# Optimization experiments

Measured on AMD Instinct MI355X. Metric: run time of the kernel, lower is better.

The kernel has to match this reference:

```python
import jax, jax.numpy as jnp
import numpy as np

N_NODES = 20000
N_EDGES = 40000
N_GRAPHS = 800
NODE_DIM = 64
EDGE_DIM = 16
ATOM = 64
CONV_DIM = 128
NUM_EMBEDS = 3   # message-passing rounds
EMB_STEPS = 3    # Set2Set processing steps
MLP1, MLP2, OUT = 512, 256, 34
BN_EPS = 1e-5


def setup_inputs() -> dict:
    key = jax.random.key(0)
    ks = jax.random.split(key, 16)
    nrm = lambda k, shape, s: jax.random.normal(k, shape, jnp.float32) * s
    inp = {}
    inp["x_feat"] = nrm(ks[0], (N_NODES, NODE_DIM), 1.0)
    inp["edge_attr"] = nrm(ks[1], (N_EDGES, EDGE_DIM), 1.0)
    inp["edge_index"] = jax.random.randint(ks[2], (2, N_EDGES), 0, N_NODES, dtype=jnp.int32)
    # sorted graph assignment; every graph non-empty (~25 nodes each)
    inp["batch"] = (jnp.arange(N_NODES) * N_GRAPHS // N_NODES).astype(jnp.int32)
    # linatoms
    inp["W_lin"] = nrm(ks[3], (NODE_DIM, ATOM), 0.1); inp["b_lin"] = jnp.zeros((ATOM,), jnp.float32)
    # edge MLP: edge_dim -> conv_dim -> atom_dim^2
    inp["W_e1"] = nrm(ks[4], (EDGE_DIM, CONV_DIM), 0.1); inp["b_e1"] = jnp.zeros((CONV_DIM,), jnp.float32)
    inp["W_e2"] = nrm(ks[5], (CONV_DIM, ATOM * ATOM), 0.02); inp["b_e2"] = jnp.zeros((ATOM * ATOM,), jnp.float32)
    inp["b_conv"] = jnp.zeros((ATOM,), jnp.float32)  # NNConv bias (root_weight=False)
    # GRU (PyTorch layout: (3*H, in), gates [r, z, n])
    inp["gru_Wih"] = nrm(ks[6], (3 * ATOM, ATOM), 0.1); inp["gru_Whh"] = nrm(ks[7], (3 * ATOM, ATOM), 0.1)
    inp["gru_bih"] = jnp.zeros((3 * ATOM,), jnp.float32); inp["gru_bhh"] = jnp.zeros((3 * ATOM,), jnp.float32)
    # Set2Set LSTM (input 2*d, hidden d; gates [i, f, g, o])
    inp["lstm_Wih"] = nrm(ks[8], (4 * ATOM, 2 * ATOM), 0.1); inp["lstm_Whh"] = nrm(ks[9], (4 * ATOM, ATOM), 0.1)
    inp["lstm_bih"] = jnp.zeros((4 * ATOM,), jnp.float32); inp["lstm_bhh"] = jnp.zeros((4 * ATOM,), jnp.float32)
    # BatchNorm1d(2*atom_dim)
    inp["bn_gamma"] = jnp.ones((2 * ATOM,), jnp.float32); inp["bn_beta"] = jnp.zeros((2 * ATOM,), jnp.float32)
    # MLP + pred head
    inp["W_m1"] = nrm(ks[10], (2 * ATOM, MLP1), 0.05); inp["b_m1"] = jnp.zeros((MLP1,), jnp.float32)
    inp["W_m2"] = nrm(ks[11], (MLP1, MLP2), 0.05); inp["b_m2"] = jnp.zeros((MLP2,), jnp.float32)
    inp["W_p"] = nrm(ks[12], (MLP2, OUT), 0.05); inp["b_p"] = jnp.zeros((OUT,), jnp.float32)
    return inp


def _forward(x_feat, edge_attr, edge_index, batch,
             W_lin, b_lin, W_e1, b_e1, W_e2, b_e2, b_conv,
             gru_Wih, gru_Whh, gru_bih, gru_bhh,
             lstm_Wih, lstm_Whh, lstm_bih, lstm_bhh,
             bn_gamma, bn_beta, W_m1, b_m1, W_m2, b_m2, W_p, b_p):
    d = ATOM
    src, dst = edge_index[0], edge_index[1]

    x = jax.nn.relu(x_feat @ W_lin + b_lin)          # [N, d]
    h = x                                            # GRU hidden state

    # edge MLP -> per-edge [d, d] weight matrices (edge_attr is constant across rounds)
    W_edges = (jax.nn.relu(edge_attr @ W_e1 + b_e1) @ W_e2 + b_e2).reshape(N_EDGES, d, d)

    deg = jax.ops.segment_sum(jnp.ones((N_EDGES,), jnp.float32), dst, num_segments=N_NODES)
    deg = jnp.maximum(deg, 1.0)[:, None]             # mean aggregation

    for _ in range(NUM_EMBEDS):
        msg = jnp.einsum('ed,edf->ef', x[src], W_edges)               # per-edge matmul
        agg = jax.ops.segment_sum(msg, dst, num_segments=N_NODES) / deg
        m = jax.nn.relu(agg + b_conv)
        # GRU cell (seq_len=1): gates ordered [r, z, n]
        gi = m @ gru_Wih.T + gru_bih
        gh = h @ gru_Whh.T + gru_bhh
        r = jax.nn.sigmoid(gi[:, :d] + gh[:, :d])
        z = jax.nn.sigmoid(gi[:, d:2 * d] + gh[:, d:2 * d])
        n = jnp.tanh(gi[:, 2 * d:] + r * gh[:, 2 * d:])
        h = (1.0 - z) * n + z * h
        x = h

    # Set2Set pooling: [N, d] -> [B, 2d]
    B = N_GRAPHS
    q_star = jnp.zeros((B, 2 * d), x.dtype)
    hl = jnp.zeros((B, d), x.dtype)
    cl = jnp.zeros((B, d), x.dtype)
    for _ in range(EMB_STEPS):
        g = q_star @ lstm_Wih.T + lstm_bih + hl @ lstm_Whh.T + lstm_bhh
        i_g = jax.nn.sigmoid(g[:, :d])
        f_g = jax.nn.sigmoid(g[:, d:2 * d])
        c_g = jnp.tanh(g[:, 2 * d:3 * d])
        o_g = jax.nn.sigmoid(g[:, 3 * d:])
        cl = f_g * cl + i_g * c_g
        hl = o_g * jnp.tanh(cl)
        q = hl                                                       # [B, d]
        e = jnp.sum(x * q[batch], axis=-1)                           # [N]
        emax = jax.ops.segment_max(e, batch, num_segments=B)
        ee = jnp.exp(e - emax[batch])
        zden = jax.ops.segment_sum(ee, batch, num_segments=B)
        a = ee / zden[batch]                                         # per-graph softmax
        r_read = jax.ops.segment_sum(a[:, None] * x, batch, num_segments=B)
        q_star = jnp.concatenate([q, r_read], axis=-1)

    # BatchNorm1d (training-mode batch stats)
    mu = jnp.mean(q_star, axis=0)
    var = jnp.var(q_star, axis=0)
    y = bn_gamma * (q_star - mu) / jnp.sqrt(var + BN_EPS) + bn_beta

    y = jax.nn.relu(y @ W_m1 + b_m1)
    y = jax.nn.relu(y @ W_m2 + b_m2)
    return y @ W_p + b_p                                             # [B, 34]


def reference(x_feat, edge_attr, edge_index, batch,
              W_lin, b_lin, W_e1, b_e1, W_e2, b_e2, b_conv,
              gru_Wih, gru_Whh, gru_bih, gru_bhh,
              lstm_Wih, lstm_Whh, lstm_bih, lstm_bhh,
              bn_gamma, bn_beta, W_m1, b_m1, W_m2, b_m2, W_p, b_p):
    return _forward(x_feat, edge_attr, edge_index, batch,
                    W_lin, b_lin, W_e1, b_e1, W_e2, b_e2, b_conv,
                    gru_Wih, gru_Whh, gru_bih, gru_bhh,
                    lstm_Wih, lstm_Whh, lstm_bih, lstm_bhh,
                    bn_gamma, bn_beta, W_m1, b_m1, W_m2, b_m2, W_p, b_p)
```

## Files before the change

### kernel.cpp

```cpp
#include <hip/hip_runtime.h>
#include <hip/hip_bf16.h>
#include <cstdint>
#include <cstddef>

#define N_NODES 20000
#define N_EDGES 40000
#define EPAD 40192
#define N_GRAPHS 800
#define ATOM 64
#define MLP1D 512
#define MLP2D 256
#define NOUT 34

typedef _Float16 h2 __attribute__((ext_vector_type(2)));
typedef _Float16 half8 __attribute__((ext_vector_type(8)));
typedef float f32x4 __attribute__((ext_vector_type(4)));
typedef float f32x16 __attribute__((ext_vector_type(16)));

__device__ __forceinline__ float sigm(float x) { return 1.f / (1.f + expf(-x)); }

#define LIN_BLKS 5000
#define HEP_BLKS (EPAD / 64)
#define BF_TOTAL (129 * 4096)
#define BF_BLKS ((BF_TOTAL + 255) / 256)
#define MISC_TOTAL (12288 + 12288 + 32768 + 16384 + EPAD + (N_GRAPHS + 1) + N_EDGES)
#define MISC_BLKS ((MISC_TOTAL + 255) / 256)
#define PREP_BLKS (LIN_BLKS + HEP_BLKS + BF_BLKS + MISC_BLKS)

__global__ __launch_bounds__(256) void prep_all(
    const float* __restrict__ x_feat, const float* __restrict__ W_lin,
    const float* __restrict__ b_lin, float* __restrict__ hx, _Float16* __restrict__ xh,
    const float* __restrict__ ea, const float* __restrict__ W_e1,
    const float* __restrict__ b_e1, _Float16* __restrict__ heT,
    const float* __restrict__ We2, const float* __restrict__ be2, _Float16* __restrict__ Bg,
    const float* __restrict__ gWih, const float* __restrict__ gWhh,
    const float* __restrict__ lWih, const float* __restrict__ lWhh,
    _Float16* __restrict__ gWihT, _Float16* __restrict__ gWhhT,
    _Float16* __restrict__ lWihT, _Float16* __restrict__ lWhhT,
    const int* __restrict__ batch, int* __restrict__ gstart,
    const int* __restrict__ dst, float* __restrict__ deg) {
    int bx = blockIdx.x;
    if (bx < LIN_BLKS) {
        __shared__ float xr[4][64];
        int ln = threadIdx.x >> 6, j = threadIdx.x & 63;
        int n = (bx << 2) + ln;
        xr[ln][j] = x_feat[(size_t)n * 64 + j];
        __syncthreads();
        float acc = b_lin[j];
        for (int i = 0; i < 64; ++i) acc = fmaf(xr[ln][i], W_lin[i * 64 + j], acc);
        float r = fmaxf(acc, 0.f);
        hx[(size_t)n * 64 + j] = r;
        xh[(size_t)n * 64 + j] = (_Float16)r;
        return;
    }
    bx -= LIN_BLKS;
    if (bx < HEP_BLKS) {
        __shared__ float eaL[64 * 17];
        int e0 = bx * 64;
        for (int idx = threadIdx.x; idx < 1024; idx += 256) {
            int r = idx >> 4, i = idx & 15;
            int e = e0 + r;
            eaL[r * 17 + i] = (e < N_EDGES) ? ea[(size_t)e * 16 + i] : 0.f;
        }
        __syncthreads();
        int w = threadIdx.x >> 6, lane = threadIdx.x & 63;
        for (int c = w; c < 128; c += 4) {
            float acc = b_e1[c];
            #pragma unroll
            for (int i = 0; i < 16; ++i)
                acc = fmaf(eaL[lane * 17 + i], W_e1[i * 128 + c], acc);
            heT[(size_t)c * EPAD + e0 + lane] = (_Float16)fmaxf(acc, 0.f);
        }
        return;
    }
    bx -= HEP_BLKS;
    if (bx < BF_BLKS) {
        int idx = bx * 256 + threadIdx.x;
        if (idx >= BF_TOTAL) return;
        int j = idx & 7, lane = (idx >> 3) & 63, ft = (idx >> 9) & 1;
        int kc = (idx >> 10) & 3, c = idx >> 12;
        int k = kc * 16 + (lane >> 5) * 8 + j;
        int f = ft * 32 + (lane & 31);
        float v = (c < 128) ? We2[(size_t)c * 4096 + k * 64 + f] : be2[k * 64 + f];
        Bg[idx] = (_Float16)v;
        return;
    }
    bx -= BF_BLKS;
    {
        int i = bx * 256 + threadIdx.x;
        if (i < 12288) { int r = i / 64, c = i % 64; gWihT[c * 192 + r] = (_Float16)gWih[i]; return; }
        i -= 12288;
        if (i < 12288) { int r = i / 64, c = i % 64; gWhhT[c * 192 + r] = (_Float16)gWhh[i]; return; }
        i -= 12288;
        if (i < 32768) { int r = i / 128, c = i % 128; lWihT[c * 256 + r] = (_Float16)lWih[i]; return; }
        i -= 32768;
        if (i < 16384) { int r = i / 64, c = i % 64; lWhhT[c * 256 + r] = (_Float16)lWhh[i]; return; }
        i -= 16384;
        if (i < EPAD) { heT[(size_t)128 * EPAD + i] = (_Float16)1.0f; return; }
        i -= EPAD;
        if (i <= N_GRAPHS) {
            if (i == N_GRAPHS) { gstart[i] = N_NODES; return; }
            int lo = 0, hi = N_NODES;
            while (lo < hi) { int mid = (lo + hi) >> 1; if (batch[mid] < i) lo = mid + 1; else hi = mid; }
            gstart[i] = lo;
            return;
        }
        i -= (N_GRAPHS + 1);
        if (i < N_EDGES) { atomicAdd(&deg[dst[i]], 1.f); return; }
    }
}

__global__ __launch_bounds__(256) void msg_v10(
    const _Float16* __restrict__ Bg, const _Float16* __restrict__ heT,
    const _Float16* __restrict__ xh, const int* __restrict__ src,
    const int* __restrict__ dst, float* __restrict__ agg)
{
    int tid = threadIdx.x;
    int w = tid >> 6, lane = tid & 63;
    int l5 = lane >> 5, l31 = lane & 31;
    int bx = blockIdx.x;
    int ft = bx & 1;
    int eg = bx >> 1;
    int m0 = eg * 128 + w * 32;
    int KS = gridDim.y, ks = blockIdx.y;
    int c0 = (129 * ks) / KS;
    int c1 = (129 * (ks + 1)) / KS;
    int nc = c1 - c0;

    union XU { h2 p[4]; half8 v; } xf[4];
    {
        int e = m0 + l31;
        const _Float16* xp = xh + (size_t)src[e] * 64 + l5 * 8;
        xf[0].v = *(const half8*)(xp);
        xf[1].v = *(const half8*)(xp + 16);
        xf[2].v = *(const half8*)(xp + 32);
        xf[3].v = *(const half8*)(xp + 48);
    }

    f32x16 acc = {};
    const _Float16* bbase = Bg + ft * 512 + lane * 8;
    const _Float16* hbase = heT + m0 + l31;

    half8 bA[4], bB[4];
    _Float16 hA, hB;

    auto LOADB = [&](int c, half8* bb, _Float16& hh) {
        const _Float16* bp = bbase + c * 4096;
        bb[0] = *(const half8*)(bp);
        bb[1] = *(const half8*)(bp + 1024);
        bb[2] = *(const half8*)(bp + 2048);
        bb[3] = *(const half8*)(bp + 3072);
        hh = hbase[c * EPAD];
    };
    auto COMP = [&](const half8* bb, _Float16 hh) {
        h2 hv = (h2){hh, hh};
        #pragma unroll
        for (int kc = 0; kc < 4; ++kc) {
            union XU a;
            #pragma unroll
            for (int j = 0; j < 4; ++j) a.p[j] = hv * xf[kc].p[j];
            acc = __builtin_amdgcn_mfma_f32_32x32x16_f16(a.v, bb[kc], acc, 0, 0, 0);
        }
    };

    int cur = bx % nc;
    LOADB(c0 + cur, bA, hA);
    int done = 1;
    for (; done + 1 < nc; done += 2) {
        int n1 = (cur + 1 == nc) ? 0 : cur + 1;
        LOADB(c0 + n1, bB, hB);
        COMP(bA, hA);
        int n2 = (n1 + 1 == nc) ? 0 : n1 + 1;
        LOADB(c0 + n2, bA, hA);
        COMP(bB, hB);
        cur = n2;
    }
    if (done < nc) {
        int n1 = (cur + 1 == nc) ? 0 : cur + 1;
        LOADB(c0 + n1, bB, hB);
        COMP(bA, hA);
        COMP(bB, hB);
    } else {
        COMP(bA, hA);
    }

    int fc = ft * 32 + l31;
    #pragma unroll
    for (int r = 0; r < 16; ++r) {
        int e = m0 + (r & 3) + 8 * (r >> 2) + 4 * l5;
        if (e < N_EDGES)
            atomicAdd(&agg[(size_t)dst[e] * 64 + fc], acc[r]);
    }
}

__global__ __launch_bounds__(256) void gru_kernel(float* __restrict__ agg,
    const float* __restrict__ deg, const float* __restrict__ bconv,
    const _Float16* __restrict__ WihT, const _Float16* __restrict__ WhhT,
    const float* __restrict__ bih, const float* __restrict__ bhh,
    float* __restrict__ hx, _Float16* __restrict__ xh) {
    __shared__ float mh[4][2][64];
    int ln = threadIdx.x >> 6, j = threadIdx.x & 63;
    int n = (blockIdx.x << 2) + ln;
    float dg = fmaxf(deg[n], 1.f);
    size_t idx = (size_t)n * 64 + j;
    float m = fmaxf(agg[idx] / dg + bconv[j], 0.f);
    agg[idx] = 0.f;
    float h = hx[idx];
    mh[ln][0][j] = m; mh[ln][1][j] = h;
    __syncthreads();
    float gri = bih[j], gzi = bih[64 + j], gni = bih[128 + j];
    float grh = bhh[j], gzh = bhh[64 + j], gnh = bhh[128 + j];
    for (int i = 0; i < 64; ++i) {
        float mi = mh[ln][0][i], hi = mh[ln][1][i];
        gri = fmaf(mi, (float)WihT[i * 192 + j], gri);
        gzi = fmaf(mi, (float)WihT[i * 192 + 64 + j], gzi);
        gni = fmaf(mi, (float)WihT[i * 192 + 128 + j], gni);
        grh = fmaf(hi, (float)WhhT[i * 192 + j], grh);
        gzh = fmaf(hi, (float)WhhT[i * 192 + 64 + j], gzh);
        gnh = fmaf(hi, (float)WhhT[i * 192 + 128 + j], gnh);
    }
    float rr = sigm(gri + grh);
    float zz = sigm(gzi + gzh);
    float nn = tanhf(gni + rr * gnh);
    float hnew = (1.f - zz) * nn + zz * h;
    hx[idx] = hnew;
    xh[idx] = (_Float16)hnew;
}

__global__ __launch_bounds__(256) void s2s_kernel(const float* __restrict__ x,
    const int* __restrict__ gstart,
    const _Float16* __restrict__ WI,
    const _Float16* __restrict__ WH,
    const float* __restrict__ bih, const float* __restrict__ bhh,
    float* __restrict__ qstar) {
    __shared__ float st[192];
    __shared__ float gl[256];
    __shared__ float redmax[4], redsum[4];
    __shared__ float raccs[4][64];
    int g = blockIdx.x, t = threadIdx.x;
    int w = t >> 6, j = t & 63;
    int s0 = gstart[g], s1 = gstart[g + 1];
    if (t < 192) st[t] = 0.f;
    float cj = 0.f;
    float bsum = bih[t] + bhh[t];
    __syncthreads();
    for (int s = 0; s < 3; ++s) {
        float a0 = bsum, a1 = 0.f;
        #pragma unroll 8
        for (int i = 0; i < 128; i += 2) {
            a0 = fmaf(st[i], (float)WI[i * 256 + t], a0);
            a1 = fmaf(st[i + 1], (float)WI[(i + 1) * 256 + t], a1);
        }
        #pragma unroll 8
        for (int i = 0; i < 64; i += 2) {
            a0 = fmaf(st[128 + i], (float)WH[i * 256 + t], a0);
            a1 = fmaf(st[128 + i + 1], (float)WH[(i + 1) * 256 + t], a1);
        }
        gl[t] = a0 + a1;
        __syncthreads();
        if (t < 64) {
            float ig = sigm(gl[t]);
            float fg = sigm(gl[64 + t]);
            float cg = tanhf(gl[128 + t]);
            float og = sigm(gl[192 + t]);
            cj = fg * cj + ig * cg;
            float hnew = og * tanhf(cj);
            st[t] = hnew;
            st[128 + t] = hnew;
        }
        __syncthreads();
        float hj = st[128 + j];
        float pmax = -3.0e38f;
        for (int n = s0 + w; n < s1; n += 4) {
            float v = x[(size_t)n * 64 + j] * hj;
            for (int o = 32; o; o >>= 1) v += __shfl_xor(v, o);
            pmax = fmaxf(pmax, v);
        }
        if (j == 0) redmax[w] = pmax;
        __syncthreads();
        float emax = fmaxf(fmaxf(redmax[0], redmax[1]), fmaxf(redmax[2], redmax[3]));
        float esum = 0.f, racc = 0.f;
        for (int n = s0 + w; n < s1; n += 4) {
            float xv = x[(size_t)n * 64 + j];
            float v = xv * hj;
            for (int o = 32; o; o >>= 1) v += __shfl_xor(v, o);
            float ww = expf(v - emax);
            esum += ww;
            racc = fmaf(ww, xv, racc);
        }
        raccs[w][j] = racc;
        if (j == 0) redsum[w] = esum;
        __syncthreads();
        if (t < 64) {
            float es = redsum[0] + redsum[1] + redsum[2] + redsum[3];
            st[64 + j] = (raccs[0][j] + raccs[1][j] + raccs[2][j] + raccs[3][j]) / es;
        }
        __syncthreads();
    }
    if (t < 64) {
        qstar[g * 128 + t] = st[t];
        qstar[g * 128 + 64 + t] = st[64 + t];
    }
}

__global__ void bn_kernel(const float* __restrict__ qs, const float* __restrict__ gamma,
                          const float* __restrict__ beta, float* __restrict__ out) {
    int c = blockIdx.x, l = threadIdx.x;
    float s = 0.f, ss = 0.f;
    for (int r = l; r < N_GRAPHS; r += 64) {
        float v = qs[r * 128 + c];
        s += v; ss += v * v;
    }
    for (int o = 32; o; o >>= 1) { s += __shfl_xor(s, o); ss += __shfl_xor(ss, o); }
    float mu = s * (1.f / N_GRAPHS);
    float var = ss * (1.f / N_GRAPHS) - mu * mu;
    float inv = rsqrtf(var + 1e-5f);
    float ga = gamma[c], be = beta[c];
    for (int r = l; r < N_GRAPHS; r += 64)
        out[r * 128 + c] = ga * (qs[r * 128 + c] - mu) * inv + be;
}

__global__ __launch_bounds__(512) void head_fused(const float* __restrict__ bno,
    const float* __restrict__ Wm1, const float* __restrict__ bm1,
    const float* __restrict__ Wm2, const float* __restrict__ bm2,
    const float* __restrict__ Wp, const float* __restrict__ bp,
    float* __restrict__ out) {
    __shared__ float row[128];
    __shared__ float y1[512];
    __shared__ float y2[256];
    int g = blockIdx.x, t = threadIdx.x;
    int rot = (g * 17) & 127;
    if (t < 128) row[t] = bno[g * 128 + t];
    __syncthreads();
    float acc = bm1[t];
    for (int s = 0; s < 128; ++s) {
        int i = (s + rot) & 127;
        acc = fmaf(row[i], Wm1[i * MLP1D + t], acc);
    }
    y1[t] = fmaxf(acc, 0.f);
    __syncthreads();
    if (t < 256) {
        float a2 = bm2[t];
        int rot2 = (g * 31) & 511;
        for (int s = 0; s < 512; ++s) {
            int i = (s + rot2) & 511;
            a2 = fmaf(y1[i], Wm2[i * MLP2D + t], a2);
        }
        y2[t] = fmaxf(a2, 0.f);
    }
    __syncthreads();
    if (t < NOUT) {
        float a3 = bp[t];
        int rot3 = (g * 13) & 255;
        for (int s = 0; s < 256; ++s) {
            int i = (s + rot3) & 255;
            a3 = fmaf(y2[i], Wp[i * NOUT + t], a3);
        }
        out[g * NOUT + t] = a3;
    }
}

extern "C" void kernel_launch(void* const* d_in, const int* in_sizes, int n_in,
                              void* d_out, int out_size, void* d_ws, size_t ws_size,
                              hipStream_t stream) {
    (void)in_sizes; (void)n_in; (void)out_size; (void)ws_size;
    const float* x_feat    = (const float*)d_in[0];
    const float* edge_attr = (const float*)d_in[1];
    const int*   eidx      = (const int*)d_in[2];
    const int*   batch     = (const int*)d_in[3];
    const float* W_lin = (const float*)d_in[4];
    const float* b_lin = (const float*)d_in[5];
    const float* W_e1  = (const float*)d_in[6];
    const float* b_e1  = (const float*)d_in[7];
    const float* W_e2  = (const float*)d_in[8];
    const float* b_e2  = (const float*)d_in[9];
    const float* b_conv= (const float*)d_in[10];
    const float* gWih  = (const float*)d_in[11];
    const float* gWhh  = (const float*)d_in[12];
    const float* gbih  = (const float*)d_in[13];
    const float* gbhh  = (const float*)d_in[14];
    const float* lWih  = (const float*)d_in[15];
    const float* lWhh  = (const float*)d_in[16];
    const float* lbih  = (const float*)d_in[17];
    const float* lbhh  = (const float*)d_in[18];
    const float* bng   = (const float*)d_in[19];
    const float* bnb   = (const float*)d_in[20];
    const float* Wm1   = (const float*)d_in[21];
    const float* bm1   = (const float*)d_in[22];
    const float* Wm2   = (const float*)d_in[23];
    const float* bm2   = (const float*)d_in[24];
    const float* Wp    = (const float*)d_in[25];
    const float* bp    = (const float*)d_in[26];
    float* out = (float*)d_out;

    const int* src = eidx;
    const int* dst = eidx + N_EDGES;

    char* w = (char*)d_ws;
    size_t off = 0;
    auto alloc = [&](size_t bytes) -> char* {
        char* p = w + off; off += (bytes + 255) & ~(size_t)255; return p;
    };
    _Float16* Bg     = (_Float16*)alloc((size_t)129 * 4096 * 2);
    _Float16* heT    = (_Float16*)alloc((size_t)129 * EPAD * 2);
    _Float16* xh     = (_Float16*)alloc((size_t)N_NODES * 64 * 2);
    float* hx        = (float*)alloc((size_t)N_NODES * 64 * 4);
    float* agg       = (float*)alloc((size_t)N_NODES * 64 * 4);
    float* deg       = (float*)alloc((size_t)N_NODES * 4);
    _Float16* gWihT  = (_Float16*)alloc(192 * 64 * 2);
    _Float16* gWhhT  = (_Float16*)alloc(192 * 64 * 2);
    _Float16* lWihT  = (_Float16*)alloc(256 * 128 * 2);
    _Float16* lWhhT  = (_Float16*)alloc(256 * 64 * 2);
    float* qstar     = (float*)alloc((size_t)N_GRAPHS * 128 * 4);
    int*   gst       = (int*)alloc((N_GRAPHS + 1) * 4);
    float* bno       = (float*)alloc((size_t)N_GRAPHS * 128 * 4);

    hipMemsetAsync(agg, 0, (size_t)N_NODES * 64 * 4 + (size_t)N_NODES * 4, stream);

    prep_all<<<PREP_BLKS, 256, 0, stream>>>(
        x_feat, W_lin, b_lin, hx, xh,
        edge_attr, W_e1, b_e1, heT,
        W_e2, b_e2, Bg,
        gWih, gWhh, lWih, lWhh, gWihT, gWhhT, lWihT, lWhhT,
        batch, gst, dst, deg);

    for (int r = 0; r < 3; ++r) {
        msg_v10<<<dim3(628, 2), 256, 0, stream>>>(Bg, heT, xh, src, dst, agg);
        gru_kernel<<<N_NODES / 4, 256, 0, stream>>>(agg, deg, b_conv, gWihT, gWhhT, gbih, gbhh, hx, xh);
    }

    s2s_kernel<<<N_GRAPHS, 256, 0, stream>>>(hx, gst, lWihT, lWhhT, lbih, lbhh, qstar);

    bn_kernel<<<128, 64, 0, stream>>>(qstar, bng, bnb, bno);
    head_fused<<<N_GRAPHS, 512, 0, stream>>>(bno, Wm1, bm1, Wm2, bm2, Wp, bp, out);
}
```

Baseline: 471.8 us.

## Restructure GRU to one thread per gate row across four nodes with fp32 float4 weights

```diff
diff --git a/kernel.cpp b/kernel.cpp
--- a/kernel.cpp
+++ b/kernel.cpp
@@ -35,8 +35,8 @@
     const float* __restrict__ We2, const float* __restrict__ be2, _Float16* __restrict__ Bg,
     const float* __restrict__ gWih, const float* __restrict__ gWhh,
     const float* __restrict__ lWih, const float* __restrict__ lWhh,
-    _Float16* __restrict__ gWihT, _Float16* __restrict__ gWhhT,
-    _Float16* __restrict__ lWihT, _Float16* __restrict__ lWhhT,
+    float* __restrict__ gWih4, float* __restrict__ gWhh4,
+    float* __restrict__ lWih4, float* __restrict__ lWhh4,
     const int* __restrict__ batch, int* __restrict__ gstart,
     const int* __restrict__ dst, float* __restrict__ deg) {
     int bx = blockIdx.x;
@@ -88,13 +88,17 @@
     bx -= BF_BLKS;
     {
         int i = bx * 256 + threadIdx.x;
-        if (i < 12288) { int r = i / 64, c = i % 64; gWihT[c * 192 + r] = (_Float16)gWih[i]; return; }
+        if (i < 12288) { int j = i & 3; int rest = i >> 2; int t = rest % 192; int ib = rest / 192;
+                         gWih4[i] = gWih[t * 64 + ib * 4 + j]; return; }
         i -= 12288;
-        if (i < 12288) { int r = i / 64, c = i % 64; gWhhT[c * 192 + r] = (_Float16)gWhh[i]; return; }
+        if (i < 12288) { int j = i & 3; int rest = i >> 2; int t = rest % 192; int ib = rest / 192;
+                         gWhh4[i] = gWhh[t * 64 + ib * 4 + j]; return; }
         i -= 12288;
-        if (i < 32768) { int r = i / 128, c = i % 128; lWihT[c * 256 + r] = (_Float16)lWih[i]; return; }
+        if (i < 32768) { int j = i & 3; int rest = i >> 2; int t = rest & 255; int ib = rest >> 8;
+                         lWih4[i] = lWih[t * 128 + ib * 4 + j]; return; }
         i -= 32768;
-        if (i < 16384) { int r = i / 64, c = i % 64; lWhhT[c * 256 + r] = (_Float16)lWhh[i]; return; }
+        if (i < 16384) { int j = i & 3; int rest = i >> 2; int t = rest & 255; int ib = rest >> 8;
+                         lWhh4[i] = lWhh[t * 64 + ib * 4 + j]; return; }
         i -= 16384;
         if (i < EPAD) { heT[(size_t)128 * EPAD + i] = (_Float16)1.0f; return; }
         i -= EPAD;
@@ -193,44 +197,66 @@
     }
 }
 
-__global__ __launch_bounds__(256) void gru_kernel(float* __restrict__ agg,
+__global__ __launch_bounds__(192) void gru_v2(float* __restrict__ agg,
     const float* __restrict__ deg, const float* __restrict__ bconv,
-    const _Float16* __restrict__ WihT, const _Float16* __restrict__ WhhT,
+    const float* __restrict__ Wih4, const float* __restrict__ Whh4,
     const float* __restrict__ bih, const float* __restrict__ bhh,
     float* __restrict__ hx, _Float16* __restrict__ xh) {
-    __shared__ float mh[4][2][64];
-    int ln = threadIdx.x >> 6, j = threadIdx.x & 63;
-    int n = (blockIdx.x << 2) + ln;
-    float dg = fmaxf(deg[n], 1.f);
-    size_t idx = (size_t)n * 64 + j;
-    float m = fmaxf(agg[idx] / dg + bconv[j], 0.f);
-    agg[idx] = 0.f;
-    float h = hx[idx];
-    mh[ln][0][j] = m; mh[ln][1][j] = h;
-    __syncthreads();
-    float gri = bih[j], gzi = bih[64 + j], gni = bih[128 + j];
-    float grh = bhh[j], gzh = bhh[64 + j], gnh = bhh[128 + j];
-    for (int i = 0; i < 64; ++i) {
-        float mi = mh[ln][0][i], hi = mh[ln][1][i];
-        gri = fmaf(mi, (float)WihT[i * 192 + j], gri);
-        gzi = fmaf(mi, (float)WihT[i * 192 + 64 + j], gzi);
-        gni = fmaf(mi, (float)WihT[i * 192 + 128 + j], gni);
-        grh = fmaf(hi, (float)WhhT[i * 192 + j], grh);
-        gzh = fmaf(hi, (float)WhhT[i * 192 + 64 + j], gzh);
-        gnh = fmaf(hi, (float)WhhT[i * 192 + 128 + j], gnh);
-    }
-    float rr = sigm(gri + grh);
-    float zz = sigm(gzi + gzh);
-    float nn = tanhf(gni + rr * gnh);
-    float hnew = (1.f - zz) * nn + zz * h;
-    hx[idx] = hnew;
-    xh[idx] = (_Float16)hnew;
+    __shared__ float mS[4][64], hS[4][64];
+    __shared__ float aI[4][192], aH[4][192];
+    int t = threadIdx.x;
+    int n0 = blockIdx.x << 2;
+    for (int idx = t; idx < 256; idx += 192) {
+        int n = idx >> 6, j = idx & 63;
+        size_t ix = (size_t)(n0 + n) * 64 + j;
+        float dg = fmaxf(deg[n0 + n], 1.f);
+        float m = fmaxf(agg[ix] / dg + bconv[j], 0.f);
+        agg[ix] = 0.f;
+        mS[n][j] = m;
+        hS[n][j] = hx[ix];
+    }
+    __syncthreads();
+    float bi = bih[t], bh = bhh[t];
+    float AI[4], AH[4];
+    #pragma unroll
+    for (int n = 0; n < 4; ++n) { AI[n] = bi; AH[n] = bh; }
+    #pragma unroll
+    for (int ib = 0; ib < 16; ++ib) {
+        f32x4 wi = *(const f32x4*)(Wih4 + ((ib * 192 + t) << 2));
+        f32x4 wh = *(const f32x4*)(Whh4 + ((ib * 192 + t) << 2));
+        int i0 = ib * 4;
+        #pragma unroll
+        for (int n = 0; n < 4; ++n) {
+            AI[n] = fmaf(mS[n][i0],     wi[0], AI[n]);
+            AI[n] = fmaf(mS[n][i0 + 1], wi[1], AI[n]);
+            AI[n] = fmaf(mS[n][i0 + 2], wi[2], AI[n]);
+            AI[n] = fmaf(mS[n][i0 + 3], wi[3], AI[n]);
+            AH[n] = fmaf(hS[n][i0],     wh[0], AH[n]);
+            AH[n] = fmaf(hS[n][i0 + 1], wh[1], AH[n]);
+            AH[n] = fmaf(hS[n][i0 + 2], wh[2], AH[n]);
+            AH[n] = fmaf(hS[n][i0 + 3], wh[3], AH[n]);
+        }
+    }
+    #pragma unroll
+    for (int n = 0; n < 4; ++n) { aI[n][t] = AI[n]; aH[n][t] = AH[n]; }
+    __syncthreads();
+    for (int idx = t; idx < 256; idx += 192) {
+        int n = idx >> 6, j = idx & 63;
+        float rr = sigm(aI[n][j] + aH[n][j]);
+        float zz = sigm(aI[n][64 + j] + aH[n][64 + j]);
+        float nn = tanhf(aI[n][128 + j] + rr * aH[n][128 + j]);
+        size_t ix = (size_t)(n0 + n) * 64 + j;
+        float h = hS[n][j];
+        float hnew = (1.f - zz) * nn + zz * h;
+        hx[ix] = hnew;
+        xh[ix] = (_Float16)hnew;
+    }
 }
 
 __global__ __launch_bounds__(256) void s2s_kernel(const float* __restrict__ x,
     const int* __restrict__ gstart,
-    const _Float16* __restrict__ WI,
-    const _Float16* __restrict__ WH,
+    const float* __restrict__ WI4,
+    const float* __restrict__ WH4,
     const float* __restrict__ bih, const float* __restrict__ bhh,
     float* __restrict__ qstar) {
     __shared__ float st[192];
@@ -245,18 +271,26 @@
     float bsum = bih[t] + bhh[t];
     __syncthreads();
     for (int s = 0; s < 3; ++s) {
-        float a0 = bsum, a1 = 0.f;
-        #pragma unroll 8
-        for (int i = 0; i < 128; i += 2) {
-            a0 = fmaf(st[i], (float)WI[i * 256 + t], a0);
-            a1 = fmaf(st[i + 1], (float)WI[(i + 1) * 256 + t], a1);
-        }
-        #pragma unroll 8
-        for (int i = 0; i < 64; i += 2) {
-            a0 = fmaf(st[128 + i], (float)WH[i * 256 + t], a0);
-            a1 = fmaf(st[128 + i + 1], (float)WH[(i + 1) * 256 + t], a1);
-        }
-        gl[t] = a0 + a1;
+        float a0 = bsum;
+        #pragma unroll
+        for (int ib = 0; ib < 32; ++ib) {
+            f32x4 wv = *(const f32x4*)(WI4 + ((ib * 256 + t) << 2));
+            int i0 = ib * 4;
+            a0 = fmaf(st[i0],     wv[0], a0);
+            a0 = fmaf(st[i0 + 1], wv[1], a0);
+            a0 = fmaf(st[i0 + 2], wv[2], a0);
+            a0 = fmaf(st[i0 + 3], wv[3], a0);
+        }
+        #pragma unroll
+        for (int ib = 0; ib < 16; ++ib) {
+            f32x4 wv = *(const f32x4*)(WH4 + ((ib * 256 + t) << 2));
+            int i0 = 128 + ib * 4;
+            a0 = fmaf(st[i0],     wv[0], a0);
+            a0 = fmaf(st[i0 + 1], wv[1], a0);
+            a0 = fmaf(st[i0 + 2], wv[2], a0);
+            a0 = fmaf(st[i0 + 3], wv[3], a0);
+        }
+        gl[t] = a0;
         __syncthreads();
         if (t < 64) {
             float ig = sigm(gl[t]);
@@ -407,10 +441,10 @@
     float* hx        = (float*)alloc((size_t)N_NODES * 64 * 4);
     float* agg       = (float*)alloc((size_t)N_NODES * 64 * 4);
     float* deg       = (float*)alloc((size_t)N_NODES * 4);
-    _Float16* gWihT  = (_Float16*)alloc(192 * 64 * 2);
-    _Float16* gWhhT  = (_Float16*)alloc(192 * 64 * 2);
-    _Float16* lWihT  = (_Float16*)alloc(256 * 128 * 2);
-    _Float16* lWhhT  = (_Float16*)alloc(256 * 64 * 2);
+    float* gWih4     = (float*)alloc(192 * 64 * 4);
+    float* gWhh4     = (float*)alloc(192 * 64 * 4);
+    float* lWih4     = (float*)alloc(256 * 128 * 4);
+    float* lWhh4     = (float*)alloc(256 * 64 * 4);
     float* qstar     = (float*)alloc((size_t)N_GRAPHS * 128 * 4);
     int*   gst       = (int*)alloc((N_GRAPHS + 1) * 4);
     float* bno       = (float*)alloc((size_t)N_GRAPHS * 128 * 4);
@@ -421,15 +455,15 @@
         x_feat, W_lin, b_lin, hx, xh,
         edge_attr, W_e1, b_e1, heT,
         W_e2, b_e2, Bg,
-        gWih, gWhh, lWih, lWhh, gWihT, gWhhT, lWihT, lWhhT,
+        gWih, gWhh, lWih, lWhh, gWih4, gWhh4, lWih4, lWhh4,
         batch, gst, dst, deg);
 
     for (int r = 0; r < 3; ++r) {
         msg_v10<<<dim3(628, 2), 256, 0, stream>>>(Bg, heT, xh, src, dst, agg);
-        gru_kernel<<<N_NODES / 4, 256, 0, stream>>>(agg, deg, b_conv, gWihT, gWhhT, gbih, gbhh, hx, xh);
-    }
-
-    s2s_kernel<<<N_GRAPHS, 256, 0, stream>>>(hx, gst, lWihT, lWhhT, lbih, lbhh, qstar);
+        gru_v2<<<N_NODES / 4, 192, 0, stream>>>(agg, deg, b_conv, gWih4, gWhh4, gbih, gbhh, hx, xh);
+    }
+
+    s2s_kernel<<<N_GRAPHS, 256, 0, stream>>>(hx, gst, lWih4, lWhh4, lbih, lbhh, qstar);
 
     bn_kernel<<<128, 64, 0, stream>>>(qstar, bng, bnb, bno);
     head_fused<<<N_GRAPHS, 512, 0, stream>>>(bno, Wm1, bm1, Wm2, bm2, Wp, bp, out);
```

Result: faster. 381.0 us, median of 2 (-19.2%).
